# Optimization experiments

Measured on AMD Instinct MI355X. Metric: run time of the kernel, lower is better.

Reference implementation:

```python
import jax, jax.numpy as jnp
import numpy as np

N_NODES = 100000
N_EDGES = 3200000
IN_DIM, HID, OUT = 5, 64, 2


def _gcn_conv(x, W, b, src, dst):
    """PyG GCNConv: out = D^-1/2 (A + I) D^-1/2 (x W) + b.
    src/dst are edge_index[0]/edge_index[1] (source_to_target flow)."""
    n = x.shape[0]
    h = x @ W  # [N, out]
    # degree including self loop: deg[i] = 1 + #edges with dst == i
    deg = jnp.ones((n,), h.dtype).at[dst].add(1.0)
    inv_sqrt = jax.lax.rsqrt(deg)
    coef = inv_sqrt[src] * inv_sqrt[dst]  # [E]
    msgs = h[src] * coef[:, None]  # [E, out] gather
    agg = jax.ops.segment_sum(msgs, dst, num_segments=n)  # scatter-add
    # self-loop contribution: norm = inv_sqrt[i]^2 = 1/deg[i]
    agg = agg + h * (1.0 / deg)[:, None]
    return agg + b


def setup_inputs() -> dict:
    key = jax.random.key(0)
    ks = jax.random.split(key, 8)
    x = jax.random.normal(ks[0], (N_NODES, IN_DIM), dtype=jnp.float32)
    edge_index = jax.random.randint(ks[1], (2, N_EDGES), 0, N_NODES, dtype=jnp.int32)
    def glorot(k, fan_in, fan_out):
        lim = np.sqrt(6.0 / (fan_in + fan_out)).astype(np.float32)
        return jax.random.uniform(k, (fan_in, fan_out), jnp.float32, -lim, lim)
    return {
        "x": x,
        "edge_index": edge_index,
        "W1": glorot(ks[2], IN_DIM, HID), "b1": jnp.zeros((HID,), jnp.float32),
        "W2": glorot(ks[3], HID, HID),    "b2": jnp.zeros((HID,), jnp.float32),
        "W3": glorot(ks[4], HID, OUT),    "b3": jnp.zeros((OUT,), jnp.float32),
    }


def reference(x, edge_index, W1, b1, W2, b2, W3, b3):
    src, dst = edge_index[0], edge_index[1]
    # eval mode: dropout is identity
    h = jax.nn.relu(_gcn_conv(x, W1, b1, src, dst))
    h = jax.nn.relu(_gcn_conv(h, W2, b2, src, dst))
    return _gcn_conv(h, W3, b3, src, dst)
```

## Files before the change

kernel.cpp:

```cpp
#include <hip/hip_runtime.h>

#define CB 256
#define MAXNB 1024


__global__ void k_hist(const int* __restrict__ dst, int* __restrict__ histG,
                       int E, int NB, int chunk) {
  __shared__ int hist[MAXNB];
  int b = blockIdx.x, tid = threadIdx.x;
  for (int k = tid; k < NB; k += 256) hist[k] = 0;
  __syncthreads();
  int beg = b * chunk, end = min(E, beg + chunk);
  int nvec = (end - beg) & ~3;
  for (int i = beg + tid * 4; i < beg + nvec; i += 1024) {
    int4 d = *(const int4*)(dst + i);
    atomicAdd(&hist[d.x >> 8], 1); atomicAdd(&hist[d.y >> 8], 1);
    atomicAdd(&hist[d.z >> 8], 1); atomicAdd(&hist[d.w >> 8], 1);
  }
  for (int i = beg + nvec + tid; i < end; i += 256) atomicAdd(&hist[dst[i] >> 8], 1);
  __syncthreads();
  for (int k = tid; k < NB; k += 256) histG[(size_t)k * CB + b] = hist[k];
}

__global__ void k_scan_local(const int* __restrict__ in, int* __restrict__ out,
                             int* __restrict__ blockSums, int n) {
  __shared__ int wsum[16];
  __shared__ int wpre[16];
  int tid = threadIdx.x;
  int gid = blockIdx.x * 1024 + tid;
  int v = (gid < n) ? in[gid] : 0;
  int lane = tid & 63, wv = tid >> 6;
  int x = v;
#pragma unroll
  for (int d = 1; d < 64; d <<= 1) {
    int t = __shfl_up(x, d);
    if (lane >= d) x += t;
  }
  if (lane == 63) wsum[wv] = x;
  __syncthreads();
  if (tid == 0) {
    int run = 0;
#pragma unroll
    for (int i = 0; i < 16; ++i) { wpre[i] = run; run += wsum[i]; }
    blockSums[blockIdx.x] = run;
  }
  __syncthreads();
  if (gid < n) out[gid] = x - v + wpre[wv];
}

__global__ void k_scan_blocks(const int* __restrict__ blockSums, int* __restrict__ blockOffs, int nb) {
  __shared__ int wtot[4];
  int tid = threadIdx.x;
  int lane = tid & 63, w = tid >> 6;
  int v = (tid < nb) ? blockSums[tid] : 0;
  int x = v;
#pragma unroll
  for (int d = 1; d < 64; d <<= 1) {
    int t = __shfl_up(x, d);
    if (lane >= d) x += t;
  }
  if (lane == 63) wtot[w] = x;
  __syncthreads();
  int pre = 0;
  for (int i = 0; i < w; ++i) pre += wtot[i];
  int ex = x - v + pre;
  if (tid < nb) blockOffs[tid] = ex;
  if (tid == nb - 1) blockOffs[nb] = ex + v;
}

__global__ void k_scatter(const int* __restrict__ src, const int* __restrict__ dst,
                          const int* __restrict__ histS, const int* __restrict__ blockOffs,
                          unsigned* __restrict__ recs, int E, int NB, int chunk) {
  __shared__ int cur[MAXNB];
  int b = blockIdx.x, tid = threadIdx.x;
  for (int k = tid; k < NB; k += 256) {
    int gid = k * CB + b;
    cur[k] = histS[gid] + blockOffs[gid >> 10];
  }
  __syncthreads();
  int beg = b * chunk, end = min(E, beg + chunk);
  int nvec = (end - beg) & ~3;
  for (int i = beg + tid * 4; i < beg + nvec; i += 1024) {
    int4 s4 = *(const int4*)(src + i);
    int4 d4 = *(const int4*)(dst + i);
    int p0 = atomicAdd(&cur[d4.x >> 8], 1);
    recs[p0] = ((unsigned)s4.x << 8) | (unsigned)(d4.x & 255);
    int p1 = atomicAdd(&cur[d4.y >> 8], 1);
    recs[p1] = ((unsigned)s4.y << 8) | (unsigned)(d4.y & 255);
    int p2 = atomicAdd(&cur[d4.z >> 8], 1);
    recs[p2] = ((unsigned)s4.z << 8) | (unsigned)(d4.z & 255);
    int p3 = atomicAdd(&cur[d4.w >> 8], 1);
    recs[p3] = ((unsigned)s4.w << 8) | (unsigned)(d4.w & 255);
  }
  for (int i = beg + nvec + tid; i < end; i += 256) {
    int s = src[i], d = dst[i];
    int pos = atomicAdd(&cur[d >> 8], 1);
    recs[pos] = ((unsigned)s << 8) | (unsigned)(d & 255);
  }
}

__global__ void k_build(const unsigned* __restrict__ recs, const int* __restrict__ histS,
                        const int* __restrict__ blockOffs, const float* __restrict__ x,
                        int* __restrict__ offs, float* __restrict__ inv_sqrt,
                        float* __restrict__ xp, int* __restrict__ srcs,
                        int N, int NB, int E) {
  __shared__ int cnt[256];
  __shared__ int cur[256];
  __shared__ int wtot[4];
  int k = blockIdx.x, tid = threadIdx.x;
  int g0 = k * CB;
  int ebeg = histS[g0] + blockOffs[g0 >> 10];
  int eend = E;
  if (k + 1 < NB) {
    int g1 = (k + 1) * CB;
    eend = histS[g1] + blockOffs[g1 >> 10];
  }
  cnt[tid] = 0;
  __syncthreads();
  int nvec = (eend - ebeg) & ~3;
  for (int i = ebeg + tid * 4; i < ebeg + nvec; i += 1024) {
    uint4 r = *(const uint4*)(recs + i);
    atomicAdd(&cnt[r.x & 255u], 1); atomicAdd(&cnt[r.y & 255u], 1);
    atomicAdd(&cnt[r.z & 255u], 1); atomicAdd(&cnt[r.w & 255u], 1);
  }
  for (int i = ebeg + nvec + tid; i < eend; i += 256) atomicAdd(&cnt[recs[i] & 255u], 1);
  __syncthreads();
  int v = cnt[tid];
  int lane = tid & 63, w = tid >> 6;
  int x_ = v;
#pragma unroll
  for (int d = 1; d < 64; d <<= 1) {
    int t = __shfl_up(x_, d);
    if (lane >= d) x_ += t;
  }
  if (lane == 63) wtot[w] = x_;
  __syncthreads();
  int pre = 0;
  for (int i = 0; i < w; ++i) pre += wtot[i];
  int gpos = ebeg + (x_ - v) + pre;
  int node = k * 256 + tid;
  if (node < N) {
    offs[node] = gpos;
    float is = rsqrtf(1.0f + (float)v);
    inv_sqrt[node] = is;
    const float* xr = x + (size_t)node * 5;
    float* xo = xp + (size_t)node * 5;
    xo[0] = xr[0] * is; xo[1] = xr[1] * is; xo[2] = xr[2] * is;
    xo[3] = xr[3] * is; xo[4] = xr[4] * is;
  }
  cur[tid] = gpos;
  if (k == NB - 1 && tid == 0) offs[N] = E;
  __syncthreads();
  for (int i = ebeg + tid * 4; i < ebeg + nvec; i += 1024) {
    uint4 r = *(const uint4*)(recs + i);
    int p0 = atomicAdd(&cur[r.x & 255u], 1); srcs[p0] = (int)(r.x >> 8);
    int p1 = atomicAdd(&cur[r.y & 255u], 1); srcs[p1] = (int)(r.y >> 8);
    int p2 = atomicAdd(&cur[r.z & 255u], 1); srcs[p2] = (int)(r.z >> 8);
    int p3 = atomicAdd(&cur[r.w & 255u], 1); srcs[p3] = (int)(r.w >> 8);
  }
  for (int i = ebeg + nvec + tid; i < eend; i += 256) {
    unsigned r = recs[i];
    int pos = atomicAdd(&cur[r & 255u], 1);
    srcs[pos] = (int)(r >> 8);
  }
}


__global__ void k_l12(const float* __restrict__ xp, const int* __restrict__ offs,
                      const int* __restrict__ srcs, const float* __restrict__ inv_sqrt,
                      const float* __restrict__ W1, const float* __restrict__ b1,
                      const float* __restrict__ W2, float* __restrict__ hp, int n) {
  __shared__ float hrow[4][2][64];
  int tid = threadIdx.x;
  int lane = tid & 63, w = tid >> 6;
  int hl = lane & 31, half = lane >> 5;
  float w1r[5];
#pragma unroll
  for (int k = 0; k < 5; ++k) w1r[k] = W1[k * 64 + lane];
  float bias = b1[lane];
  float wreg[64];
#pragma unroll
  for (int k = 0; k < 64; ++k) wreg[k] = W2[k * 64 + lane];
  float* slotA = &hrow[w][0][0];
  float* slotB = &hrow[w][1][0];
  int wid0 = (blockIdx.x * blockDim.x + tid) >> 6;
  int nw = (gridDim.x * blockDim.x) >> 6;
  for (int i2 = wid0 * 2; i2 < n; i2 += nw * 2) {
    int iA = i2, iB = i2 + 1;
    int node = (half == 0) ? iA : iB;
    bool valid = node < n;
    float a0 = 0.f, a1 = 0.f, a2 = 0.f, a3 = 0.f, a4 = 0.f;
    float isd = 0.f;
    if (valid) {
      isd = inv_sqrt[node];
      int beg = offs[node], end = offs[node + 1];
      for (int j = beg + hl; j < end; j += 32) {
        int s = srcs[j];
        const float* xs = xp + (size_t)s * 5;
        float4 xv = *(const float4*)xs;
        float x4 = xs[4];
        a0 += xv.x; a1 += xv.y; a2 += xv.z; a3 += xv.w; a4 += x4;
      }
    }
#pragma unroll
    for (int d = 16; d; d >>= 1) {
      a0 += __shfl_xor(a0, d); a1 += __shfl_xor(a1, d); a2 += __shfl_xor(a2, d);
      a3 += __shfl_xor(a3, d); a4 += __shfl_xor(a4, d);
    }
    if (valid) {
      const float* xi = xp + (size_t)node * 5;
      a0 = (a0 + xi[0]) * isd; a1 = (a1 + xi[1]) * isd; a2 = (a2 + xi[2]) * isd;
      a3 = (a3 + xi[3]) * isd; a4 = (a4 + xi[4]) * isd;
    }
    float aA0 = __shfl(a0, hl),      aA1 = __shfl(a1, hl),      aA2 = __shfl(a2, hl);
    float aA3 = __shfl(a3, hl),      aA4 = __shfl(a4, hl);
    float aB0 = __shfl(a0, hl | 32), aB1 = __shfl(a1, hl | 32), aB2 = __shfl(a2, hl | 32);
    float aB3 = __shfl(a3, hl | 32), aB4 = __shfl(a4, hl | 32);
    float isdA = __shfl(isd, 0), isdB = __shfl(isd, 32);
    float hA = bias;
    hA = fmaf(aA0, w1r[0], hA); hA = fmaf(aA1, w1r[1], hA); hA = fmaf(aA2, w1r[2], hA);
    hA = fmaf(aA3, w1r[3], hA); hA = fmaf(aA4, w1r[4], hA);
    hA = fmaxf(hA, 0.f);
    float hB = bias;
    hB = fmaf(aB0, w1r[0], hB); hB = fmaf(aB1, w1r[1], hB); hB = fmaf(aB2, w1r[2], hB);
    hB = fmaf(aB3, w1r[3], hB); hB = fmaf(aB4, w1r[4], hB);
    hB = fmaxf(hB, 0.f);
    slotA[lane] = hA;
    slotB[lane] = hB;
    float ac0 = 0.f, ac1 = 0.f, ac2 = 0.f, ac3 = 0.f;
#pragma unroll
    for (int k4 = 0; k4 < 16; ++k4) {
      float4 hq = *(const float4*)&slotA[k4 * 4];
      ac0 = fmaf(hq.x, wreg[k4 * 4],     ac0);
      ac1 = fmaf(hq.y, wreg[k4 * 4 + 1], ac1);
      ac2 = fmaf(hq.z, wreg[k4 * 4 + 2], ac2);
      ac3 = fmaf(hq.w, wreg[k4 * 4 + 3], ac3);
    }
    hp[(size_t)iA * 64 + lane] = ((ac0 + ac1) + (ac2 + ac3)) * isdA;
    if (iB < n) {
      float bc0 = 0.f, bc1 = 0.f, bc2 = 0.f, bc3 = 0.f;
#pragma unroll
      for (int k4 = 0; k4 < 16; ++k4) {
        float4 hq = *(const float4*)&slotB[k4 * 4];
        bc0 = fmaf(hq.x, wreg[k4 * 4],     bc0);
        bc1 = fmaf(hq.y, wreg[k4 * 4 + 1], bc1);
        bc2 = fmaf(hq.z, wreg[k4 * 4 + 2], bc2);
        bc3 = fmaf(hq.w, wreg[k4 * 4 + 3], bc3);
      }
      hp[(size_t)iB * 64 + lane] = ((bc0 + bc1) + (bc2 + bc3)) * isdB;
    }
  }
}

__global__ void k_agg64w3(const float* __restrict__ hp, const int* __restrict__ offs,
                          const int* __restrict__ srcs, const float* __restrict__ inv_sqrt,
                          const float* __restrict__ b2, const float* __restrict__ W3,
                          float* __restrict__ h3p, int n) {
  int wid = (blockIdx.x * blockDim.x + threadIdx.x) >> 6;
  int lane = threadIdx.x & 63;
  if (wid >= n) return;
  int sub = lane >> 4;
  int fl  = lane & 15;
  float w30[4], w31[4];
#pragma unroll
  for (int q = 0; q < 4; ++q) {
    w30[q] = W3[(fl * 4 + q) * 2];
    w31[q] = W3[(fl * 4 + q) * 2 + 1];
  }
  int beg = offs[wid], end = offs[wid + 1];
  float isd = inv_sqrt[wid];
  float ax0 = 0.f, ay0 = 0.f, az0 = 0.f, aw0 = 0.f;
  float ax1 = 0.f, ay1 = 0.f, az1 = 0.f, aw1 = 0.f;
  int c = beg;
  for (; c + 16 <= end; c += 16) {
    int j = c + (sub << 2);
    int4 sv = *(const int4*)(srcs + j);
    float4 r0 = *(const float4*)(hp + (size_t)sv.x * 64 + fl * 4);
    float4 r1 = *(const float4*)(hp + (size_t)sv.y * 64 + fl * 4);
    float4 r2 = *(const float4*)(hp + (size_t)sv.z * 64 + fl * 4);
    float4 r3 = *(const float4*)(hp + (size_t)sv.w * 64 + fl * 4);
    ax0 += r0.x; ay0 += r0.y; az0 += r0.z; aw0 += r0.w;
    ax1 += r1.x; ay1 += r1.y; az1 += r1.z; aw1 += r1.w;
    ax0 += r2.x; ay0 += r2.y; az0 += r2.z; aw0 += r2.w;
    ax1 += r3.x; ay1 += r3.y; az1 += r3.z; aw1 += r3.w;
  }
  for (int j = c + sub; j < end; j += 4) {
    int s0 = srcs[j];
    float4 r0 = *(const float4*)(hp + (size_t)s0 * 64 + fl * 4);
    ax0 += r0.x; ay0 += r0.y; az0 += r0.z; aw0 += r0.w;
  }
  float ax = ax0 + ax1, ay = ay0 + ay1, az = az0 + az1, aw = aw0 + aw1;
  ax += __shfl_xor(ax, 16); ay += __shfl_xor(ay, 16);
  az += __shfl_xor(az, 16); aw += __shfl_xor(aw, 16);
  ax += __shfl_xor(ax, 32); ay += __shfl_xor(ay, 32);
  az += __shfl_xor(az, 32); aw += __shfl_xor(aw, 32);
  float4 self = *(const float4*)(hp + (size_t)wid * 64 + fl * 4);
  float4 bb   = *(const float4*)(b2 + fl * 4);
  float hx = fmaxf(fmaf(isd, ax + self.x, bb.x), 0.f);
  float hy = fmaxf(fmaf(isd, ay + self.y, bb.y), 0.f);
  float hz = fmaxf(fmaf(isd, az + self.z, bb.z), 0.f);
  float hw = fmaxf(fmaf(isd, aw + self.w, bb.w), 0.f);
  float p0 = hx * w30[0] + hy * w30[1] + hz * w30[2] + hw * w30[3];
  float p1 = hx * w31[0] + hy * w31[1] + hz * w31[2] + hw * w31[3];
#pragma unroll
  for (int d = 8; d; d >>= 1) { p0 += __shfl_xor(p0, d); p1 += __shfl_xor(p1, d); }
  if (lane == 0) {
    h3p[(size_t)wid * 2]     = p0 * isd;
    h3p[(size_t)wid * 2 + 1] = p1 * isd;
  }
}

__global__ void k_agg2(const float* __restrict__ h3p, const int* __restrict__ offs,
                       const int* __restrict__ srcs, const float* __restrict__ inv_sqrt,
                       const float* __restrict__ b3, float* __restrict__ out, int n) {
  int wv = (blockIdx.x * blockDim.x + threadIdx.x) >> 6;
  int lane = threadIdx.x & 63;
  int half = lane >> 5, hl = lane & 31;
  int node = wv * 2 + half;
  float a0 = 0.f, a1 = 0.f;
  if (node < n) {
    int beg = offs[node], end = offs[node + 1];
    for (int j = beg + hl; j < end; j += 32) {
      int s = srcs[j];
      float2 hv = *(const float2*)(h3p + (size_t)s * 2);
      a0 += hv.x; a1 += hv.y;
    }
  }
#pragma unroll
  for (int d = 16; d; d >>= 1) { a0 += __shfl_xor(a0, d); a1 += __shfl_xor(a1, d); }
  if (node < n && hl == 0) {
    float isd = inv_sqrt[node];
    float2 self = *(const float2*)(h3p + (size_t)node * 2);
    out[(size_t)node * 2]     = fmaf(isd, a0 + self.x, b3[0]);
    out[(size_t)node * 2 + 1] = fmaf(isd, a1 + self.y, b3[1]);
  }
}


extern "C" void kernel_launch(void* const* d_in, const int* in_sizes, int n_in,
                              void* d_out, int out_size, void* d_ws, size_t ws_size,
                              hipStream_t stream) {
  const float* x  = (const float*)d_in[0];
  const int*   ei = (const int*)d_in[1];
  const float* W1 = (const float*)d_in[2];
  const float* b1 = (const float*)d_in[3];
  const float* W2 = (const float*)d_in[4];
  const float* b2 = (const float*)d_in[5];
  const float* W3 = (const float*)d_in[6];
  const float* b3 = (const float*)d_in[7];
  float* out = (float*)d_out;

  const int N = in_sizes[0] / 5;
  const int E = in_sizes[1] / 2;
  const int* src = ei;
  const int* dst = ei + E;

  const int NB = (N + 255) >> 8;
  const int chunk = (E + CB - 1) / CB;
  const int n2 = NB * CB;
  const int nb2 = (n2 + 1023) / 1024;

  char* p = (char*)d_ws;
  auto alloc = [&](size_t bytes) {
    char* r = p;
    p += (bytes + 255) & ~(size_t)255;
    return r;
  };
  int*      histG     = (int*)alloc((size_t)n2 * 4);
  int*      histS     = (int*)alloc((size_t)n2 * 4);
  int*      blockSums = (int*)alloc((size_t)nb2 * 4);
  int*      blockOffs = (int*)alloc((size_t)(nb2 + 1) * 4);
  unsigned* recs      = (unsigned*)alloc((size_t)E * 4);
  int*      srcs      = (int*)alloc((size_t)E * 4);
  int*      offs      = (int*)alloc((size_t)(N + 1) * 4);
  float*    inv_sqrt  = (float*)alloc((size_t)N * 4);
  float*    xp        = (float*)alloc((size_t)N * 5 * 4);
  float*    hp        = (float*)alloc((size_t)N * 64 * 4);
  float*    h3p       = (float*)alloc((size_t)N * 2 * 4);

  const int wavesBlocks = (N * 64 + 255) / 256;
  const int pairs = (N + 1) / 2;
  const int pairBlocks = (pairs * 64 + 255) / 256;

  k_hist<<<CB, 256, 0, stream>>>(dst, histG, E, NB, chunk);
  k_scan_local<<<nb2, 1024, 0, stream>>>(histG, histS, blockSums, n2);
  k_scan_blocks<<<1, 256, 0, stream>>>(blockSums, blockOffs, nb2);
  k_scatter<<<CB, 256, 0, stream>>>(src, dst, histS, blockOffs, recs, E, NB, chunk);
  k_build<<<NB, 256, 0, stream>>>(recs, histS, blockOffs, x, offs, inv_sqrt, xp, srcs, N, NB, E);

  k_l12<<<2048, 256, 0, stream>>>(xp, offs, srcs, inv_sqrt, W1, b1, W2, hp, N);
  k_agg64w3<<<wavesBlocks, 256, 0, stream>>>(hp, offs, srcs, inv_sqrt, b2, W3, h3p, N);
  k_agg2<<<pairBlocks, 256, 0, stream>>>(h3p, offs, srcs, inv_sqrt, b3, out, N);
}
```

Before: 226.1 us.

## Move W2 matmul after layer-2 aggregation and persist the aggregation kernel

Layer 1 now writes the normalized relu(h1) rows, and the 64x64 W2 multiply moves into the layer-2 aggregation kernel, applied once per node after the neighbor sum (aggregate-then-transform). The aggregation kernel becomes a grid-stride persistent kernel with 2048 blocks that loads W2 into registers once per thread and reuses it across nodes. The gather traffic stays the same and the matmul count per node is unchanged, but the W2 register load and LDS staging leave the layer-1 kernel. The cost is higher register pressure in the gather-bound kernel, which may reduce occupancy and latency hiding.

```diff
diff --git a/kernel.cpp b/kernel.cpp
--- a/kernel.cpp
+++ b/kernel.cpp
@@ -166,23 +166,17 @@
 }
 
 
-__global__ void k_l12(const float* __restrict__ xp, const int* __restrict__ offs,
-                      const int* __restrict__ srcs, const float* __restrict__ inv_sqrt,
-                      const float* __restrict__ W1, const float* __restrict__ b1,
-                      const float* __restrict__ W2, float* __restrict__ hp, int n) {
-  __shared__ float hrow[4][2][64];
+__global__ void k_l1(const float* __restrict__ xp, const int* __restrict__ offs,
+                     const int* __restrict__ srcs, const float* __restrict__ inv_sqrt,
+                     const float* __restrict__ W1, const float* __restrict__ b1,
+                     float* __restrict__ h1p, int n) {
   int tid = threadIdx.x;
-  int lane = tid & 63, w = tid >> 6;
+  int lane = tid & 63;
   int hl = lane & 31, half = lane >> 5;
   float w1r[5];
 #pragma unroll
   for (int k = 0; k < 5; ++k) w1r[k] = W1[k * 64 + lane];
   float bias = b1[lane];
-  float wreg[64];
-#pragma unroll
-  for (int k = 0; k < 64; ++k) wreg[k] = W2[k * 64 + lane];
-  float* slotA = &hrow[w][0][0];
-  float* slotB = &hrow[w][1][0];
   int wid0 = (blockIdx.x * blockDim.x + tid) >> 6;
   int nw = (gridDim.x * blockDim.x) >> 6;
   for (int i2 = wid0 * 2; i2 < n; i2 += nw * 2) {
@@ -220,93 +214,85 @@
     float hA = bias;
     hA = fmaf(aA0, w1r[0], hA); hA = fmaf(aA1, w1r[1], hA); hA = fmaf(aA2, w1r[2], hA);
     hA = fmaf(aA3, w1r[3], hA); hA = fmaf(aA4, w1r[4], hA);
-    hA = fmaxf(hA, 0.f);
-    float hB = bias;
-    hB = fmaf(aB0, w1r[0], hB); hB = fmaf(aB1, w1r[1], hB); hB = fmaf(aB2, w1r[2], hB);
-    hB = fmaf(aB3, w1r[3], hB); hB = fmaf(aB4, w1r[4], hB);
-    hB = fmaxf(hB, 0.f);
-    slotA[lane] = hA;
-    slotB[lane] = hB;
-    float ac0 = 0.f, ac1 = 0.f, ac2 = 0.f, ac3 = 0.f;
-#pragma unroll
-    for (int k4 = 0; k4 < 16; ++k4) {
-      float4 hq = *(const float4*)&slotA[k4 * 4];
-      ac0 = fmaf(hq.x, wreg[k4 * 4],     ac0);
-      ac1 = fmaf(hq.y, wreg[k4 * 4 + 1], ac1);
-      ac2 = fmaf(hq.z, wreg[k4 * 4 + 2], ac2);
-      ac3 = fmaf(hq.w, wreg[k4 * 4 + 3], ac3);
-    }
-    hp[(size_t)iA * 64 + lane] = ((ac0 + ac1) + (ac2 + ac3)) * isdA;
+    h1p[(size_t)iA * 64 + lane] = fmaxf(hA, 0.f) * isdA;
     if (iB < n) {
-      float bc0 = 0.f, bc1 = 0.f, bc2 = 0.f, bc3 = 0.f;
-#pragma unroll
-      for (int k4 = 0; k4 < 16; ++k4) {
-        float4 hq = *(const float4*)&slotB[k4 * 4];
-        bc0 = fmaf(hq.x, wreg[k4 * 4],     bc0);
-        bc1 = fmaf(hq.y, wreg[k4 * 4 + 1], bc1);
-        bc2 = fmaf(hq.z, wreg[k4 * 4 + 2], bc2);
-        bc3 = fmaf(hq.w, wreg[k4 * 4 + 3], bc3);
-      }
-      hp[(size_t)iB * 64 + lane] = ((bc0 + bc1) + (bc2 + bc3)) * isdB;
-    }
-  }
-}
-
-__global__ void k_agg64w3(const float* __restrict__ hp, const int* __restrict__ offs,
+      float hB = bias;
+      hB = fmaf(aB0, w1r[0], hB); hB = fmaf(aB1, w1r[1], hB); hB = fmaf(aB2, w1r[2], hB);
+      hB = fmaf(aB3, w1r[3], hB); hB = fmaf(aB4, w1r[4], hB);
+      h1p[(size_t)iB * 64 + lane] = fmaxf(hB, 0.f) * isdB;
+    }
+  }
+}
+
+__global__ void k_agg64w3(const float* __restrict__ h1p, const int* __restrict__ offs,
                           const int* __restrict__ srcs, const float* __restrict__ inv_sqrt,
-                          const float* __restrict__ b2, const float* __restrict__ W3,
-                          float* __restrict__ h3p, int n) {
-  int wid = (blockIdx.x * blockDim.x + threadIdx.x) >> 6;
-  int lane = threadIdx.x & 63;
-  if (wid >= n) return;
+                          const float* __restrict__ W2, const float* __restrict__ b2,
+                          const float* __restrict__ W3, float* __restrict__ h3p, int n) {
+  __shared__ float aggrow[4][68];
+  int tid = threadIdx.x;
+  int lane = tid & 63, w = tid >> 6;
+  float wreg[64];
+#pragma unroll
+  for (int k = 0; k < 64; ++k) wreg[k] = W2[k * 64 + lane];
+  float w30 = W3[lane * 2], w31 = W3[lane * 2 + 1];
+  float b2v = b2[lane];
+  float* slot = &aggrow[w][0];
   int sub = lane >> 4;
   int fl  = lane & 15;
-  float w30[4], w31[4];
-#pragma unroll
-  for (int q = 0; q < 4; ++q) {
-    w30[q] = W3[(fl * 4 + q) * 2];
-    w31[q] = W3[(fl * 4 + q) * 2 + 1];
-  }
-  int beg = offs[wid], end = offs[wid + 1];
-  float isd = inv_sqrt[wid];
-  float ax0 = 0.f, ay0 = 0.f, az0 = 0.f, aw0 = 0.f;
-  float ax1 = 0.f, ay1 = 0.f, az1 = 0.f, aw1 = 0.f;
-  int c = beg;
-  for (; c + 16 <= end; c += 16) {
-    int j = c + (sub << 2);
-    int4 sv = *(const int4*)(srcs + j);
-    float4 r0 = *(const float4*)(hp + (size_t)sv.x * 64 + fl * 4);
-    float4 r1 = *(const float4*)(hp + (size_t)sv.y * 64 + fl * 4);
-    float4 r2 = *(const float4*)(hp + (size_t)sv.z * 64 + fl * 4);
-    float4 r3 = *(const float4*)(hp + (size_t)sv.w * 64 + fl * 4);
-    ax0 += r0.x; ay0 += r0.y; az0 += r0.z; aw0 += r0.w;
-    ax1 += r1.x; ay1 += r1.y; az1 += r1.z; aw1 += r1.w;
-    ax0 += r2.x; ay0 += r2.y; az0 += r2.z; aw0 += r2.w;
-    ax1 += r3.x; ay1 += r3.y; az1 += r3.z; aw1 += r3.w;
-  }
-  for (int j = c + sub; j < end; j += 4) {
-    int s0 = srcs[j];
-    float4 r0 = *(const float4*)(hp + (size_t)s0 * 64 + fl * 4);
-    ax0 += r0.x; ay0 += r0.y; az0 += r0.z; aw0 += r0.w;
-  }
-  float ax = ax0 + ax1, ay = ay0 + ay1, az = az0 + az1, aw = aw0 + aw1;
-  ax += __shfl_xor(ax, 16); ay += __shfl_xor(ay, 16);
-  az += __shfl_xor(az, 16); aw += __shfl_xor(aw, 16);
-  ax += __shfl_xor(ax, 32); ay += __shfl_xor(ay, 32);
-  az += __shfl_xor(az, 32); aw += __shfl_xor(aw, 32);
-  float4 self = *(const float4*)(hp + (size_t)wid * 64 + fl * 4);
-  float4 bb   = *(const float4*)(b2 + fl * 4);
-  float hx = fmaxf(fmaf(isd, ax + self.x, bb.x), 0.f);
-  float hy = fmaxf(fmaf(isd, ay + self.y, bb.y), 0.f);
-  float hz = fmaxf(fmaf(isd, az + self.z, bb.z), 0.f);
-  float hw = fmaxf(fmaf(isd, aw + self.w, bb.w), 0.f);
-  float p0 = hx * w30[0] + hy * w30[1] + hz * w30[2] + hw * w30[3];
-  float p1 = hx * w31[0] + hy * w31[1] + hz * w31[2] + hw * w31[3];
-#pragma unroll
-  for (int d = 8; d; d >>= 1) { p0 += __shfl_xor(p0, d); p1 += __shfl_xor(p1, d); }
-  if (lane == 0) {
-    h3p[(size_t)wid * 2]     = p0 * isd;
-    h3p[(size_t)wid * 2 + 1] = p1 * isd;
+  int wid0 = (blockIdx.x * blockDim.x + tid) >> 6;
+  int nw = (gridDim.x * blockDim.x) >> 6;
+  for (int i = wid0; i < n; i += nw) {
+    int beg = offs[i], end = offs[i + 1];
+    float isd = inv_sqrt[i];
+    float ax0 = 0.f, ay0 = 0.f, az0 = 0.f, aw0 = 0.f;
+    float ax1 = 0.f, ay1 = 0.f, az1 = 0.f, aw1 = 0.f;
+    int c = beg;
+    for (; c + 16 <= end; c += 16) {
+      int j = c + (sub << 2);
+      int4 sv = *(const int4*)(srcs + j);
+      float4 r0 = *(const float4*)(h1p + (size_t)sv.x * 64 + fl * 4);
+      float4 r1 = *(const float4*)(h1p + (size_t)sv.y * 64 + fl * 4);
+      float4 r2 = *(const float4*)(h1p + (size_t)sv.z * 64 + fl * 4);
+      float4 r3 = *(const float4*)(h1p + (size_t)sv.w * 64 + fl * 4);
+      ax0 += r0.x; ay0 += r0.y; az0 += r0.z; aw0 += r0.w;
+      ax1 += r1.x; ay1 += r1.y; az1 += r1.z; aw1 += r1.w;
+      ax0 += r2.x; ay0 += r2.y; az0 += r2.z; aw0 += r2.w;
+      ax1 += r3.x; ay1 += r3.y; az1 += r3.z; aw1 += r3.w;
+    }
+    for (int j = c + sub; j < end; j += 4) {
+      int s0 = srcs[j];
+      float4 r0 = *(const float4*)(h1p + (size_t)s0 * 64 + fl * 4);
+      ax0 += r0.x; ay0 += r0.y; az0 += r0.z; aw0 += r0.w;
+    }
+    float ax = ax0 + ax1, ay = ay0 + ay1, az = az0 + az1, aw = aw0 + aw1;
+    ax += __shfl_xor(ax, 16); ay += __shfl_xor(ay, 16);
+    az += __shfl_xor(az, 16); aw += __shfl_xor(aw, 16);
+    ax += __shfl_xor(ax, 32); ay += __shfl_xor(ay, 32);
+    az += __shfl_xor(az, 32); aw += __shfl_xor(aw, 32);
+    float4 self = *(const float4*)(h1p + (size_t)i * 64 + fl * 4);
+    ax += self.x; ay += self.y; az += self.z; aw += self.w;
+    if (sub == 0) {
+      float4 q; q.x = ax; q.y = ay; q.z = az; q.w = aw;
+      *(float4*)&slot[fl * 4] = q;
+    }
+    float z0 = 0.f, z1 = 0.f, z2 = 0.f, z3 = 0.f;
+#pragma unroll
+    for (int k4 = 0; k4 < 16; ++k4) {
+      float4 q = *(const float4*)&slot[k4 * 4];
+      z0 = fmaf(q.x, wreg[k4 * 4],     z0);
+      z1 = fmaf(q.y, wreg[k4 * 4 + 1], z1);
+      z2 = fmaf(q.z, wreg[k4 * 4 + 2], z2);
+      z3 = fmaf(q.w, wreg[k4 * 4 + 3], z3);
+    }
+    float z = (z0 + z1) + (z2 + z3);
+    float h2 = fmaxf(fmaf(isd, z, b2v), 0.f);
+    float p0 = h2 * w30, p1 = h2 * w31;
+#pragma unroll
+    for (int d = 32; d; d >>= 1) { p0 += __shfl_xor(p0, d); p1 += __shfl_xor(p1, d); }
+    if (lane == 0) {
+      h3p[(size_t)i * 2]     = p0 * isd;
+      h3p[(size_t)i * 2 + 1] = p1 * isd;
+    }
   }
 }
 
@@ -378,7 +364,6 @@
   float*    hp        = (float*)alloc((size_t)N * 64 * 4);
   float*    h3p       = (float*)alloc((size_t)N * 2 * 4);
 
-  const int wavesBlocks = (N * 64 + 255) / 256;
   const int pairs = (N + 1) / 2;
   const int pairBlocks = (pairs * 64 + 255) / 256;
 
@@ -388,7 +373,7 @@
   k_scatter<<<CB, 256, 0, stream>>>(src, dst, histS, blockOffs, recs, E, NB, chunk);
   k_build<<<NB, 256, 0, stream>>>(recs, histS, blockOffs, x, offs, inv_sqrt, xp, srcs, N, NB, E);
 
-  k_l12<<<2048, 256, 0, stream>>>(xp, offs, srcs, inv_sqrt, W1, b1, W2, hp, N);
-  k_agg64w3<<<wavesBlocks, 256, 0, stream>>>(hp, offs, srcs, inv_sqrt, b2, W3, h3p, N);
+  k_l1<<<2048, 256, 0, stream>>>(xp, offs, srcs, inv_sqrt, W1, b1, hp, N);
+  k_agg64w3<<<2048, 256, 0, stream>>>(hp, offs, srcs, inv_sqrt, W2, b2, W3, h3p, N);
   k_agg2<<<pairBlocks, 256, 0, stream>>>(h3p, offs, srcs, inv_sqrt, b3, out, N);
 }
```

Result: no change. 225.4 us (-0.3%).

## Split layer-2 features into 8-wide slices for cache-local gather aggregation

Applied to the files above, without the earlier changes.

Layer-2 projected features are written in a slice-major layout of eight 8-float slices. The neighbor aggregation now runs per slice, so each slice's gathered working set is small enough to stay cached instead of scattering across the full 64-wide rows. The old fused aggregate-plus-W3 kernel is split into a slice aggregation kernel and a finishing kernel that applies bias, ReLU and the W3 projection. The split adds a full N×64 intermediate write and read and one extra kernel launch.

```diff
diff --git a/kernel.cpp b/kernel.cpp
--- a/kernel.cpp
+++ b/kernel.cpp
@@ -169,11 +169,12 @@
 __global__ void k_l12(const float* __restrict__ xp, const int* __restrict__ offs,
                       const int* __restrict__ srcs, const float* __restrict__ inv_sqrt,
                       const float* __restrict__ W1, const float* __restrict__ b1,
-                      const float* __restrict__ W2, float* __restrict__ hp, int n) {
+                      const float* __restrict__ W2, float* __restrict__ hS, int n) {
   __shared__ float hrow[4][2][64];
   int tid = threadIdx.x;
   int lane = tid & 63, w = tid >> 6;
   int hl = lane & 31, half = lane >> 5;
+  int slice = lane >> 3, feat = lane & 7;
   float w1r[5];
 #pragma unroll
   for (int k = 0; k < 5; ++k) w1r[k] = W1[k * 64 + lane];
@@ -236,7 +237,7 @@
       ac2 = fmaf(hq.z, wreg[k4 * 4 + 2], ac2);
       ac3 = fmaf(hq.w, wreg[k4 * 4 + 3], ac3);
     }
-    hp[(size_t)iA * 64 + lane] = ((ac0 + ac1) + (ac2 + ac3)) * isdA;
+    hS[((size_t)slice * n + iA) * 8 + feat] = ((ac0 + ac1) + (ac2 + ac3)) * isdA;
     if (iB < n) {
       float bc0 = 0.f, bc1 = 0.f, bc2 = 0.f, bc3 = 0.f;
 #pragma unroll
@@ -247,66 +248,63 @@
         bc2 = fmaf(hq.z, wreg[k4 * 4 + 2], bc2);
         bc3 = fmaf(hq.w, wreg[k4 * 4 + 3], bc3);
       }
-      hp[(size_t)iB * 64 + lane] = ((bc0 + bc1) + (bc2 + bc3)) * isdB;
-    }
-  }
-}
-
-__global__ void k_agg64w3(const float* __restrict__ hp, const int* __restrict__ offs,
-                          const int* __restrict__ srcs, const float* __restrict__ inv_sqrt,
-                          const float* __restrict__ b2, const float* __restrict__ W3,
-                          float* __restrict__ h3p, int n) {
-  int wid = (blockIdx.x * blockDim.x + threadIdx.x) >> 6;
+      hS[((size_t)slice * n + iB) * 8 + feat] = ((bc0 + bc1) + (bc2 + bc3)) * isdB;
+    }
+  }
+}
+
+__global__ void k_aggS(const float* __restrict__ hS, const int* __restrict__ offs,
+                       const int* __restrict__ srcs, float* __restrict__ h2agg, int n) {
+  int slice = blockIdx.x & 7;
+  int tid = threadIdx.x;
+  int lane = tid & 63;
+  int slot = lane >> 3, feat = lane & 7;
+  const float* hbase = hS + (size_t)slice * n * 8;
+  int wid0 = ((blockIdx.x >> 3) << 2) + (tid >> 6);
+  int nw = (gridDim.x >> 3) << 2;
+  for (int i = wid0; i < n; i += nw) {
+    int beg = offs[i], end = offs[i + 1];
+    float a0 = 0.f, a1 = 0.f, a2 = 0.f, a3 = 0.f;
+    int c = beg;
+    for (; c + 32 <= end; c += 32) {
+      int j = c + (slot << 2);
+      int4 sv = *(const int4*)(srcs + j);
+      a0 += hbase[(size_t)sv.x * 8 + feat];
+      a1 += hbase[(size_t)sv.y * 8 + feat];
+      a2 += hbase[(size_t)sv.z * 8 + feat];
+      a3 += hbase[(size_t)sv.w * 8 + feat];
+    }
+    int j0 = c + (slot << 2);
+    int je = min(j0 + 4, end);
+    for (int j = j0; j < je; ++j) a0 += hbase[(size_t)srcs[j] * 8 + feat];
+    float acc = (a0 + a1) + (a2 + a3);
+    acc += __shfl_xor(acc, 8);
+    acc += __shfl_xor(acc, 16);
+    acc += __shfl_xor(acc, 32);
+    acc += hbase[(size_t)i * 8 + feat];
+    if (slot == 0) h2agg[(size_t)i * 64 + slice * 8 + feat] = acc;
+  }
+}
+
+__global__ void k_fin(const float* __restrict__ h2agg, const float* __restrict__ inv_sqrt,
+                      const float* __restrict__ b2, const float* __restrict__ W3,
+                      float* __restrict__ h3p, int n) {
   int lane = threadIdx.x & 63;
-  if (wid >= n) return;
-  int sub = lane >> 4;
-  int fl  = lane & 15;
-  float w30[4], w31[4];
-#pragma unroll
-  for (int q = 0; q < 4; ++q) {
-    w30[q] = W3[(fl * 4 + q) * 2];
-    w31[q] = W3[(fl * 4 + q) * 2 + 1];
-  }
-  int beg = offs[wid], end = offs[wid + 1];
-  float isd = inv_sqrt[wid];
-  float ax0 = 0.f, ay0 = 0.f, az0 = 0.f, aw0 = 0.f;
-  float ax1 = 0.f, ay1 = 0.f, az1 = 0.f, aw1 = 0.f;
-  int c = beg;
-  for (; c + 16 <= end; c += 16) {
-    int j = c + (sub << 2);
-    int4 sv = *(const int4*)(srcs + j);
-    float4 r0 = *(const float4*)(hp + (size_t)sv.x * 64 + fl * 4);
-    float4 r1 = *(const float4*)(hp + (size_t)sv.y * 64 + fl * 4);
-    float4 r2 = *(const float4*)(hp + (size_t)sv.z * 64 + fl * 4);
-    float4 r3 = *(const float4*)(hp + (size_t)sv.w * 64 + fl * 4);
-    ax0 += r0.x; ay0 += r0.y; az0 += r0.z; aw0 += r0.w;
-    ax1 += r1.x; ay1 += r1.y; az1 += r1.z; aw1 += r1.w;
-    ax0 += r2.x; ay0 += r2.y; az0 += r2.z; aw0 += r2.w;
-    ax1 += r3.x; ay1 += r3.y; az1 += r3.z; aw1 += r3.w;
-  }
-  for (int j = c + sub; j < end; j += 4) {
-    int s0 = srcs[j];
-    float4 r0 = *(const float4*)(hp + (size_t)s0 * 64 + fl * 4);
-    ax0 += r0.x; ay0 += r0.y; az0 += r0.z; aw0 += r0.w;
-  }
-  float ax = ax0 + ax1, ay = ay0 + ay1, az = az0 + az1, aw = aw0 + aw1;
-  ax += __shfl_xor(ax, 16); ay += __shfl_xor(ay, 16);
-  az += __shfl_xor(az, 16); aw += __shfl_xor(aw, 16);
-  ax += __shfl_xor(ax, 32); ay += __shfl_xor(ay, 32);
-  az += __shfl_xor(az, 32); aw += __shfl_xor(aw, 32);
-  float4 self = *(const float4*)(hp + (size_t)wid * 64 + fl * 4);
-  float4 bb   = *(const float4*)(b2 + fl * 4);
-  float hx = fmaxf(fmaf(isd, ax + self.x, bb.x), 0.f);
-  float hy = fmaxf(fmaf(isd, ay + self.y, bb.y), 0.f);
-  float hz = fmaxf(fmaf(isd, az + self.z, bb.z), 0.f);
-  float hw = fmaxf(fmaf(isd, aw + self.w, bb.w), 0.f);
-  float p0 = hx * w30[0] + hy * w30[1] + hz * w30[2] + hw * w30[3];
-  float p1 = hx * w31[0] + hy * w31[1] + hz * w31[2] + hw * w31[3];
-#pragma unroll
-  for (int d = 8; d; d >>= 1) { p0 += __shfl_xor(p0, d); p1 += __shfl_xor(p1, d); }
-  if (lane == 0) {
-    h3p[(size_t)wid * 2]     = p0 * isd;
-    h3p[(size_t)wid * 2 + 1] = p1 * isd;
+  float b2v = b2[lane];
+  float w30 = W3[lane * 2], w31 = W3[lane * 2 + 1];
+  int wid0 = (blockIdx.x * blockDim.x + threadIdx.x) >> 6;
+  int nw = (gridDim.x * blockDim.x) >> 6;
+  for (int i = wid0; i < n; i += nw) {
+    float isd = inv_sqrt[i];
+    float agg = h2agg[(size_t)i * 64 + lane];
+    float h2 = fmaxf(fmaf(isd, agg, b2v), 0.f);
+    float p0 = h2 * w30, p1 = h2 * w31;
+#pragma unroll
+    for (int d = 32; d; d >>= 1) { p0 += __shfl_xor(p0, d); p1 += __shfl_xor(p1, d); }
+    if (lane == 0) {
+      h3p[(size_t)i * 2]     = p0 * isd;
+      h3p[(size_t)i * 2 + 1] = p1 * isd;
+    }
   }
 }
 
@@ -375,10 +373,10 @@
   int*      offs      = (int*)alloc((size_t)(N + 1) * 4);
   float*    inv_sqrt  = (float*)alloc((size_t)N * 4);
   float*    xp        = (float*)alloc((size_t)N * 5 * 4);
-  float*    hp        = (float*)alloc((size_t)N * 64 * 4);
+  float*    hS        = (float*)alloc((size_t)N * 64 * 4);
+  float*    h2agg     = (float*)alloc((size_t)N * 64 * 4);
   float*    h3p       = (float*)alloc((size_t)N * 2 * 4);
 
-  const int wavesBlocks = (N * 64 + 255) / 256;
   const int pairs = (N + 1) / 2;
   const int pairBlocks = (pairs * 64 + 255) / 256;
 
@@ -388,7 +386,8 @@
   k_scatter<<<CB, 256, 0, stream>>>(src, dst, histS, blockOffs, recs, E, NB, chunk);
   k_build<<<NB, 256, 0, stream>>>(recs, histS, blockOffs, x, offs, inv_sqrt, xp, srcs, N, NB, E);
 
-  k_l12<<<2048, 256, 0, stream>>>(xp, offs, srcs, inv_sqrt, W1, b1, W2, hp, N);
-  k_agg64w3<<<wavesBlocks, 256, 0, stream>>>(hp, offs, srcs, inv_sqrt, b2, W3, h3p, N);
+  k_l12<<<2048, 256, 0, stream>>>(xp, offs, srcs, inv_sqrt, W1, b1, W2, hS, N);
+  k_aggS<<<2048, 256, 0, stream>>>(hS, offs, srcs, h2agg, N);
+  k_fin<<<2048, 256, 0, stream>>>(h2agg, inv_sqrt, b2, W3, h3p, N);
   k_agg2<<<pairBlocks, 256, 0, stream>>>(h3p, offs, srcs, inv_sqrt, b3, out, N);
 }
```

Result: slower. 413.3 us (+82.8%).
